# Kernel tuning notes

Measured on AMD Instinct MI355X. Metric: run time of the kernel, lower is better.

The kernel has to match this reference:

```python
import jax, jax.numpy as jnp
import numpy as np
from math import sqrt

H = 16  # head_num


def setup_inputs() -> dict:
    key = jax.random.key(0)
    ks = jax.random.split(key, 8)
    B, Sq, Skv, Dq, Dkv, Dall = 2, 2048, 2048, 1024, 1024, 1024
    x = jax.random.normal(ks[0], (B, Sq, Dq), dtype=jnp.float32)
    y = jax.random.normal(ks[1], (B, Skv, Dkv), dtype=jnp.float32)
    attention_mask = jnp.ones((B, 1, Sq, Skv), dtype=jnp.int32)
    # torch nn.Linear weights are [out, in]
    Wq = jax.random.normal(ks[2], (Dall, Dq), dtype=jnp.float32) * 0.02
    Wk = jax.random.normal(ks[3], (Dall, Dkv), dtype=jnp.float32) * 0.02
    Wv = jax.random.normal(ks[4], (Dall, Dkv), dtype=jnp.float32) * 0.02
    Wo = jax.random.normal(ks[5], (Dq, Dall), dtype=jnp.float32) * 0.02
    bo = jnp.zeros((Dq,), dtype=jnp.float32)
    return {"x": x, "y": y, "attention_mask": attention_mask,
            "Wq": Wq, "Wk": Wk, "Wv": Wv, "Wo": Wo, "bo": bo}


def reference(x, y, attention_mask, Wq, Wk, Wv, Wo, bo):
    B, Sq, _ = x.shape
    Dall = Wq.shape[0]
    Dh = Dall // H
    # projections (torch Linear: x @ W.T), split heads -> [B, H, S, Dh]
    q = (x @ Wq.T).reshape(B, Sq, H, Dh).transpose(0, 2, 1, 3)
    k = (y @ Wk.T).reshape(B, -1, H, Dh).transpose(0, 2, 1, 3)
    v = (y @ Wv.T).reshape(B, -1, H, Dh).transpose(0, 2, 1, 3)
    scores = jnp.einsum('bhqd,bhkd->bhqk', q, k)  # [B,H,Sq,Skv]
    mask = (attention_mask == 0)  # masked_fill where mask.eq(0) -> but torch does mask.eq(0) then fills True positions
    scores = jnp.where(mask, jnp.float32(-1e9), scores)
    # NOTE: faithful quirk - mask applied before scaling; scale uses sqrt(h_size)
    attn = jax.nn.softmax(scores / sqrt(Dh), axis=-1)
    out = jnp.einsum('bhqk,bhkd->bhqd', attn, v)
    out = out.transpose(0, 2, 1, 3).reshape(B, Sq, Dall)
    return out @ Wo.T + bo
```

## Files before the change

kernel.cpp:

```cpp
#include <hip/hip_runtime.h>
#include <stdint.h>


typedef __attribute__((ext_vector_type(8))) short bf16x8;
typedef __attribute__((ext_vector_type(4))) float f32x4;
typedef __attribute__((ext_vector_type(16))) float f32x16;
typedef __attribute__((ext_vector_type(2))) unsigned int u32x2;

#define LOG2E 1.44269504088896f
#define QSCALE (0.125f * LOG2E)

static __device__ __forceinline__ unsigned short f2bf(float f) {
  union { float f; unsigned int u; } v; v.f = f;
  unsigned int r = v.u + 0x7FFFu + ((v.u >> 16) & 1u);
  return (unsigned short)(r >> 16);
}

static __device__ __forceinline__ void g2l16(const void* gsrc, void* ldst) {
  __builtin_amdgcn_global_load_lds((const __attribute__((address_space(1))) unsigned int*)gsrc,
                                   (__attribute__((address_space(3))) unsigned int*)ldst,
                                   16, 0, 0);
}

static __device__ __forceinline__ unsigned int cvt_pk_bf16(float lo, float hi) {
  unsigned int r;
  asm("v_cvt_pk_bf16_f32 %0, %1, %2" : "=v"(r) : "v"(lo), "v"(hi));
  return r;
}

static __device__ __forceinline__ u32x2 pl32swap(unsigned int a, unsigned int b) {
  return __builtin_amdgcn_permlane32_swap(a, b, false, false);
}

static __device__ __forceinline__ f32x16 mfma32(bf16x8 a, bf16x8 b, f32x16 c) {
  return __builtin_amdgcn_mfma_f32_32x32x16_bf16(a, b, c, 0, 0, 0);
}

static __device__ __forceinline__ size_t kfrag_addr(int row, int col) {
  int b = row >> 11, s = row & 2047;
  int h = col >> 6, d = col & 63;
  int t32 = s >> 5, r31 = s & 31;
  int ks = d >> 4, r5 = (d >> 3) & 1, e = d & 7;
  return (size_t)(b * 16 + h) * 131072 + (size_t)t32 * 2048 + ks * 512 + (r5 * 32 + r31) * 8 + e;
}
static __device__ __forceinline__ size_t vfrag_addr(int row, int col) {
  int b = row >> 11, s = row & 2047;
  int h = col >> 6, d = col & 63;
  int t64 = s >> 6, k2 = (s >> 4) & 3, r5 = (s >> 3) & 1, e = s & 7;
  int mb = d >> 5, r31 = d & 31;
  return (size_t)(b * 16 + h) * 131072 + (size_t)t64 * 4096 + (mb * 4 + k2) * 512 + (r5 * 32 + r31) * 8 + e;
}

__global__ void k_prep(const float* __restrict__ x, const float* __restrict__ y,
                       const float* __restrict__ Wq, const float* __restrict__ Wk,
                       const float* __restrict__ Wv, const float* __restrict__ Wo,
                       const int* __restrict__ mask,
                       unsigned short* __restrict__ xb, unsigned short* __restrict__ yb,
                       unsigned short* __restrict__ Wqb, unsigned short* __restrict__ Wkb,
                       unsigned short* __restrict__ Wvb, unsigned short* __restrict__ Wob,
                       unsigned long long* __restrict__ bits, unsigned int* __restrict__ flag) {
  const int task = blockIdx.y;
  if (task == 6) {
    const int lane = threadIdx.x & 63;
    int gw = blockIdx.x * 4 + (threadIdx.x >> 6);
    bool any0 = false;
    for (; gw < 131072; gw += 4096) {
      int m = mask[(size_t)gw * 64 + lane];
      unsigned long long bal = __ballot(m != 0);
      if (lane == 0) {
        bits[gw] = bal;
        any0 |= (bal != ~0ull);
      }
    }
    if (lane == 0 && any0) atomicAnd(flag, 0u);
    return;
  }
  const float* in; unsigned short* out; int n;
  switch (task) {
    case 0: in = x;  out = xb;  n = 4194304; break;
    case 1: in = y;  out = yb;  n = 4194304; break;
    case 2: in = Wq; out = Wqb; n = 1048576; break;
    case 3: in = Wk; out = Wkb; n = 1048576; break;
    case 4: in = Wv; out = Wvb; n = 1048576; break;
    default: in = Wo; out = Wob; n = 1048576; break;
  }
  int i = (blockIdx.x * blockDim.x + threadIdx.x) * 4;
  const int stride = gridDim.x * blockDim.x * 4;
  for (; i < n; i += stride) {
    float4 v = *reinterpret_cast<const float4*>(in + i);
    ushort4 o;
    o.x = f2bf(v.x); o.y = f2bf(v.y); o.z = f2bf(v.z); o.w = f2bf(v.w);
    *reinterpret_cast<ushort4*>(out + i) = o;
  }
}

template <int OM>
static __device__ __forceinline__ void gemm_body(const unsigned short* __restrict__ A,
                                                 const unsigned short* __restrict__ W,
                                                 void* __restrict__ Cout,
                                                 const float* __restrict__ bias,
                                                 float scale) {
  __shared__ __align__(16) unsigned short As[128 * 32];
  __shared__ __align__(16) unsigned short Bs[128 * 32];
  const int tid = threadIdx.x;
  const int w = tid >> 6, lane = tid & 63;
  const int wr = w >> 1, wc = w & 1;
  const int l15 = lane & 15, lg = lane >> 4;
  const int bm = blockIdx.x, bn = blockIdx.y;

  f32x4 acc[4][4] = {};

  const int e0 = w * 1024 + lane * 8;
  const int e1 = e0 + 512;
  const int r0 = e0 >> 5, c0 = e0 & 31;
  const int r1 = e1 >> 5, c1 = e1 & 31;
  const unsigned short* A0 = A + (size_t)(bm * 128 + r0) * 1024 + c0;
  const unsigned short* A1 = A + (size_t)(bm * 128 + r1) * 1024 + c1;
  const unsigned short* W0 = W + (size_t)(bn * 128 + r0) * 1024 + c0;
  const unsigned short* W1 = W + (size_t)(bn * 128 + r1) * 1024 + c1;

  for (int kt = 0; kt < 1024; kt += 32) {
    g2l16(A0 + kt, (char*)As + e0 * 2);
    g2l16(A1 + kt, (char*)As + e1 * 2);
    g2l16(W0 + kt, (char*)Bs + e0 * 2);
    g2l16(W1 + kt, (char*)Bs + e1 * 2);
    __syncthreads();
    bf16x8 a[4], b[4];
#pragma unroll
    for (int mi = 0; mi < 4; ++mi)
      a[mi] = *reinterpret_cast<const bf16x8*>(As + (wr * 64 + mi * 16 + l15) * 32 + lg * 8);
#pragma unroll
    for (int ni = 0; ni < 4; ++ni)
      b[ni] = *reinterpret_cast<const bf16x8*>(Bs + (wc * 64 + ni * 16 + l15) * 32 + lg * 8);
#pragma unroll
    for (int mi = 0; mi < 4; ++mi)
#pragma unroll
      for (int ni = 0; ni < 4; ++ni)
        acc[mi][ni] = __builtin_amdgcn_mfma_f32_16x16x32_bf16(a[mi], b[ni], acc[mi][ni], 0, 0, 0);
    __syncthreads();
  }

#pragma unroll
  for (int ni = 0; ni < 4; ++ni) {
    const int gcol = bn * 128 + wc * 64 + ni * 16 + l15;
    float bv = (OM == 1) ? bias[gcol] : 0.f;
#pragma unroll
    for (int mi = 0; mi < 4; ++mi) {
#pragma unroll
      for (int r = 0; r < 4; ++r) {
        const int grow = bm * 128 + wr * 64 + mi * 16 + lg * 4 + r;
        if (OM == 0)
          ((unsigned short*)Cout)[(size_t)grow * 1024 + gcol] = f2bf(acc[mi][ni][r]);
        else if (OM == 1)
          ((float*)Cout)[(size_t)grow * 1024 + gcol] = acc[mi][ni][r] + bv;
        else if (OM == 2)
          ((unsigned short*)Cout)[kfrag_addr(grow, gcol)] = f2bf(acc[mi][ni][r] * scale);
        else
          ((unsigned short*)Cout)[vfrag_addr(grow, gcol)] = f2bf(acc[mi][ni][r]);
      }
    }
  }
}

__global__ __launch_bounds__(256) void k_gemm_qkv(
    const unsigned short* __restrict__ xb, const unsigned short* __restrict__ yb,
    const unsigned short* __restrict__ Wq, const unsigned short* __restrict__ Wk,
    const unsigned short* __restrict__ Wv,
    unsigned short* __restrict__ Qf, unsigned short* __restrict__ Kf,
    unsigned short* __restrict__ Vf) {
  const int z = blockIdx.z;
  if (z == 0) gemm_body<2>(xb, Wq, Qf, nullptr, QSCALE);
  else if (z == 1) gemm_body<2>(yb, Wk, Kf, nullptr, 1.f);
  else gemm_body<3>(yb, Wv, Vf, nullptr, 1.f);
}

__global__ __launch_bounds__(256) void k_gemm_o(
    const unsigned short* __restrict__ AO, const unsigned short* __restrict__ Wo,
    float* __restrict__ out, const float* __restrict__ bo) {
  gemm_body<1>(AO, Wo, out, bo, 1.f);
}


#define BUILD_PB2(SP, K2, IDX) {                                   \
    unsigned int c0_ = cvt_pk_bf16(SP[(K2)*8 + 0], SP[(K2)*8 + 1]);\
    unsigned int c1_ = cvt_pk_bf16(SP[(K2)*8 + 2], SP[(K2)*8 + 3]);\
    unsigned int c2_ = cvt_pk_bf16(SP[(K2)*8 + 4], SP[(K2)*8 + 5]);\
    unsigned int c3_ = cvt_pk_bf16(SP[(K2)*8 + 6], SP[(K2)*8 + 7]);\
    u32x2 r0_ = pl32swap(c0_, c2_);                                \
    u32x2 r1_ = pl32swap(c1_, c3_);                                \
    union { unsigned int u[4]; bf16x8 v; } f_;                     \
    f_.u[0] = r0_.x; f_.u[1] = r1_.x; f_.u[2] = r0_.y; f_.u[3] = r1_.y; \
    pb[IDX] = f_.v; }

#define STAGE_TILE(T, BUF) {                                                  \
    const size_t toff_ = (size_t)(T) * 8192;                                  \
    char* kb_ = smem + (BUF) * 16384;                                         \
    const int o0_ = (w * 2 + 0) * 1024 + lane * 16;                           \
    const int o1_ = (w * 2 + 1) * 1024 + lane * 16;                           \
    g2l16(Kg + toff_ + o0_, kb_ + o0_);                                       \
    g2l16(Kg + toff_ + o1_, kb_ + o1_);                                       \
    g2l16(Vg + toff_ + o0_, kb_ + 8192 + o0_);                                \
    g2l16(Vg + toff_ + o1_, kb_ + 8192 + o1_);                                \
  }

__global__ __launch_bounds__(256, 2) void k_attn(
    const unsigned short* __restrict__ Qf, const unsigned short* __restrict__ Kf,
    const unsigned short* __restrict__ Vf, const unsigned long long* __restrict__ bits,
    const unsigned int* __restrict__ flag, unsigned short* __restrict__ AO) {
  __shared__ __align__(16) char smem[32768];
  const int tid = threadIdx.x, w = tid >> 6, lane = tid & 63;
  const int l31 = lane & 31, hi = lane >> 5;
  const int bid = blockIdx.x;
  const int xcd = bid & 7, rr = bid >> 3;
  const int j = rr & 15;
  const int g = xcd + ((rr >> 4) << 3);
  const int h = g & 15, b = g >> 4;
  const int q = j * 128 + w * 32 + l31;
  const bool allfull = (*flag == 0xFFFFFFFFu);
  const f32x16 z16 = {};

  const size_t bh = (size_t)(b * 16 + h) * 131072;
  bf16x8 qf[4];
  const unsigned short* Qp = Qf + bh + (size_t)(j * 4 + w) * 2048 + lane * 8;
#pragma unroll
  for (int ks = 0; ks < 4; ++ks)
    qf[ks] = *reinterpret_cast<const bf16x8*>(Qp + ks * 512);

  const char* Kg = (const char*)(Kf + bh);
  const char* Vg = (const char*)(Vf + bh);
  const unsigned long long* brow = bits + (size_t)(b * 2048 + q) * 32;

  f32x16 o0 = {}, o1 = {};
  float l_run = 0.f;

  STAGE_TILE(0, 0)
  __syncthreads();

  for (int t = 0; t < 32; ++t) {
    const int cur = t & 1;
    if (t < 31) STAGE_TILE(t + 1, cur ^ 1)
    const char* Kb = smem + cur * 16384;
    const char* Vb = Kb + 8192;

    bf16x8 kf[8], vf[8];
#pragma unroll
    for (int f = 0; f < 8; ++f)
      kf[f] = *reinterpret_cast<const bf16x8*>(Kb + f * 1024 + lane * 16);

    f32x16 s0 = z16, s1 = z16;
#pragma unroll
    for (int ks = 0; ks < 4; ++ks) {
      s0 = mfma32(kf[ks], qf[ks], s0);
      s1 = mfma32(kf[4 + ks], qf[ks], s1);
    }

#pragma unroll
    for (int f = 0; f < 8; ++f)
      vf[f] = *reinterpret_cast<const bf16x8*>(Vb + f * 1024 + lane * 16);

    if (!allfull) {
      unsigned long long wb = brow[t];
      if (!__all(wb == ~0ull)) {
#pragma unroll
        for (int r = 0; r < 16; ++r) {
          const int kl = (r & 3) + 8 * (r >> 2) + 4 * hi;
          s0[r] = ((wb >> kl) & 1ull) ? s0[r] : -1e9f;
          s1[r] = ((wb >> (kl + 32)) & 1ull) ? s1[r] : -1e9f;
        }
      }
    }

#pragma unroll
    for (int r = 0; r < 16; ++r) {
      s0[r] = __builtin_amdgcn_exp2f(s0[r]);
      s1[r] = __builtin_amdgcn_exp2f(s1[r]);
    }
    {
      float sm[8];
#pragma unroll
      for (int r = 0; r < 8; ++r) sm[r] = (s0[r] + s0[r + 8]) + (s1[r] + s1[r + 8]);
      sm[0] += sm[4]; sm[1] += sm[5]; sm[2] += sm[6]; sm[3] += sm[7];
      sm[0] += sm[2]; sm[1] += sm[3];
      float ls = sm[0] + sm[1];
      u32x2 sw = pl32swap(__builtin_bit_cast(unsigned int, ls),
                          __builtin_bit_cast(unsigned int, ls));
      l_run += __builtin_bit_cast(float, sw.x) + __builtin_bit_cast(float, sw.y);
    }

    bf16x8 pb[4];
    BUILD_PB2(s0, 0, 0) BUILD_PB2(s0, 1, 1) BUILD_PB2(s1, 0, 2) BUILD_PB2(s1, 1, 3)
#pragma unroll
    for (int k2 = 0; k2 < 4; ++k2) {
      o0 = mfma32(vf[k2], pb[k2], o0);
      o1 = mfma32(vf[4 + k2], pb[k2], o1);
    }
    __syncthreads();
  }

  const float inv = 1.f / l_run;
  unsigned short* Orow = AO + (size_t)(b * 2048 + q) * 1024 + h * 64;
#pragma unroll
  for (int g2 = 0; g2 < 4; ++g2) {
    ushort4 pk;
    pk.x = f2bf(o0[g2 * 4 + 0] * inv);
    pk.y = f2bf(o0[g2 * 4 + 1] * inv);
    pk.z = f2bf(o0[g2 * 4 + 2] * inv);
    pk.w = f2bf(o0[g2 * 4 + 3] * inv);
    *reinterpret_cast<ushort4*>(Orow + 8 * g2 + 4 * hi) = pk;
    pk.x = f2bf(o1[g2 * 4 + 0] * inv);
    pk.y = f2bf(o1[g2 * 4 + 1] * inv);
    pk.z = f2bf(o1[g2 * 4 + 2] * inv);
    pk.w = f2bf(o1[g2 * 4 + 3] * inv);
    *reinterpret_cast<ushort4*>(Orow + 32 + 8 * g2 + 4 * hi) = pk;
  }
}

extern "C" void kernel_launch(void* const* d_in, const int* in_sizes, int n_in,
                              void* d_out, int out_size, void* d_ws, size_t ws_size,
                              hipStream_t stream) {
  const float* x  = (const float*)d_in[0];
  const float* y  = (const float*)d_in[1];
  const int* mask = (const int*)d_in[2];
  const float* Wq = (const float*)d_in[3];
  const float* Wk = (const float*)d_in[4];
  const float* Wv = (const float*)d_in[5];
  const float* Wo = (const float*)d_in[6];
  const float* bo = (const float*)d_in[7];

  char* ws = (char*)d_ws;
  const size_t MB = 1ull << 20;
  unsigned short* xb  = (unsigned short*)(ws + 0 * MB);
  unsigned short* yb  = (unsigned short*)(ws + 8 * MB);
  unsigned short* Wqb = (unsigned short*)(ws + 16 * MB);
  unsigned short* Wkb = (unsigned short*)(ws + 18 * MB);
  unsigned short* Wvb = (unsigned short*)(ws + 20 * MB);
  unsigned short* Wob = (unsigned short*)(ws + 22 * MB);
  unsigned short* Qf  = (unsigned short*)(ws + 24 * MB);
  unsigned short* Kf  = (unsigned short*)(ws + 32 * MB);
  unsigned short* Vf  = (unsigned short*)(ws + 40 * MB);
  unsigned short* AOb = (unsigned short*)(ws + 56 * MB);
  unsigned long long* bits = (unsigned long long*)(ws + 64 * MB);
  unsigned int* flag = (unsigned int*)(ws + 65 * MB);

  hipMemsetAsync(flag, 0xFF, 4, stream);
  k_prep<<<dim3(1024, 7), 256, 0, stream>>>(x, y, Wq, Wk, Wv, Wo, mask,
                                            xb, yb, Wqb, Wkb, Wvb, Wob, bits, flag);
  k_gemm_qkv<<<dim3(32, 8, 3), 256, 0, stream>>>(xb, yb, Wqb, Wkb, Wvb, Qf, Kf, Vf);
  k_attn<<<512, 256, 0, stream>>>(Qf, Kf, Vf, bits, flag, AOb);
  k_gemm_o<<<dim3(32, 8, 1), 256, 0, stream>>>(AOb, Wob, (float*)d_out, bo);
}
```

Before: 131.1 us.

## Fuse K and V projections sharing A tile; shrink output GEMM M-tile

K and V projections now run in one block that loads the shared y tile once and multiplies it against both Wk and Wv, removing a redundant A-tile load and one third of the QKV grid. Each KV block holds two accumulator sets, which raises register pressure and can cut occupancy. The output projection now uses 64x128 tiles with each wave covering 32 columns, doubling the grid to 512 blocks so the CUs are better filled.

```diff
diff --git a/kernel.cpp b/kernel.cpp
--- a/kernel.cpp
+++ b/kernel.cpp
@@ -94,14 +94,10 @@
   }
 }
 
-template <int OM>
-static __device__ __forceinline__ void gemm_body(const unsigned short* __restrict__ A,
-                                                 const unsigned short* __restrict__ W,
-                                                 void* __restrict__ Cout,
-                                                 const float* __restrict__ bias,
-                                                 float scale) {
-  __shared__ __align__(16) unsigned short As[128 * 32];
-  __shared__ __align__(16) unsigned short Bs[128 * 32];
+static __device__ __forceinline__ void gemm_q_core(
+    const unsigned short* __restrict__ A, const unsigned short* __restrict__ W,
+    unsigned short* __restrict__ Cout, float scale,
+    unsigned short* As, unsigned short* Bs) {
   const int tid = threadIdx.x;
   const int w = tid >> 6, lane = tid & 63;
   const int wr = w >> 1, wc = w & 1;
@@ -143,20 +139,78 @@
 #pragma unroll
   for (int ni = 0; ni < 4; ++ni) {
     const int gcol = bn * 128 + wc * 64 + ni * 16 + l15;
-    float bv = (OM == 1) ? bias[gcol] : 0.f;
 #pragma unroll
     for (int mi = 0; mi < 4; ++mi) {
 #pragma unroll
       for (int r = 0; r < 4; ++r) {
         const int grow = bm * 128 + wr * 64 + mi * 16 + lg * 4 + r;
-        if (OM == 0)
-          ((unsigned short*)Cout)[(size_t)grow * 1024 + gcol] = f2bf(acc[mi][ni][r]);
-        else if (OM == 1)
-          ((float*)Cout)[(size_t)grow * 1024 + gcol] = acc[mi][ni][r] + bv;
-        else if (OM == 2)
-          ((unsigned short*)Cout)[kfrag_addr(grow, gcol)] = f2bf(acc[mi][ni][r] * scale);
-        else
-          ((unsigned short*)Cout)[vfrag_addr(grow, gcol)] = f2bf(acc[mi][ni][r]);
+        Cout[kfrag_addr(grow, gcol)] = f2bf(acc[mi][ni][r] * scale);
+      }
+    }
+  }
+}
+
+static __device__ __forceinline__ void gemm_kv_core(
+    const unsigned short* __restrict__ A, const unsigned short* __restrict__ Wk,
+    const unsigned short* __restrict__ Wv,
+    unsigned short* __restrict__ Kf, unsigned short* __restrict__ Vf,
+    unsigned short* As, unsigned short* B0s, unsigned short* B1s) {
+  const int tid = threadIdx.x;
+  const int w = tid >> 6, lane = tid & 63;
+  const int wr = w >> 1, wc = w & 1;
+  const int l15 = lane & 15, lg = lane >> 4;
+  const int bm = blockIdx.x, bn = blockIdx.y;
+
+  f32x4 acck[4][4] = {}, accv[4][4] = {};
+
+  const int e0 = w * 1024 + lane * 8;
+  const int e1 = e0 + 512;
+  const int r0 = e0 >> 5, c0 = e0 & 31;
+  const int r1 = e1 >> 5, c1 = e1 & 31;
+  const unsigned short* A0 = A + (size_t)(bm * 128 + r0) * 1024 + c0;
+  const unsigned short* A1 = A + (size_t)(bm * 128 + r1) * 1024 + c1;
+  const unsigned short* K0 = Wk + (size_t)(bn * 128 + r0) * 1024 + c0;
+  const unsigned short* K1 = Wk + (size_t)(bn * 128 + r1) * 1024 + c1;
+  const unsigned short* V0 = Wv + (size_t)(bn * 128 + r0) * 1024 + c0;
+  const unsigned short* V1 = Wv + (size_t)(bn * 128 + r1) * 1024 + c1;
+
+  for (int kt = 0; kt < 1024; kt += 32) {
+    g2l16(A0 + kt, (char*)As + e0 * 2);
+    g2l16(A1 + kt, (char*)As + e1 * 2);
+    g2l16(K0 + kt, (char*)B0s + e0 * 2);
+    g2l16(K1 + kt, (char*)B0s + e1 * 2);
+    g2l16(V0 + kt, (char*)B1s + e0 * 2);
+    g2l16(V1 + kt, (char*)B1s + e1 * 2);
+    __syncthreads();
+    bf16x8 a[4], bk[4], bv[4];
+#pragma unroll
+    for (int mi = 0; mi < 4; ++mi)
+      a[mi] = *reinterpret_cast<const bf16x8*>(As + (wr * 64 + mi * 16 + l15) * 32 + lg * 8);
+#pragma unroll
+    for (int ni = 0; ni < 4; ++ni) {
+      bk[ni] = *reinterpret_cast<const bf16x8*>(B0s + (wc * 64 + ni * 16 + l15) * 32 + lg * 8);
+      bv[ni] = *reinterpret_cast<const bf16x8*>(B1s + (wc * 64 + ni * 16 + l15) * 32 + lg * 8);
+    }
+#pragma unroll
+    for (int mi = 0; mi < 4; ++mi)
+#pragma unroll
+      for (int ni = 0; ni < 4; ++ni) {
+        acck[mi][ni] = __builtin_amdgcn_mfma_f32_16x16x32_bf16(a[mi], bk[ni], acck[mi][ni], 0, 0, 0);
+        accv[mi][ni] = __builtin_amdgcn_mfma_f32_16x16x32_bf16(a[mi], bv[ni], accv[mi][ni], 0, 0, 0);
+      }
+    __syncthreads();
+  }
+
+#pragma unroll
+  for (int ni = 0; ni < 4; ++ni) {
+    const int gcol = bn * 128 + wc * 64 + ni * 16 + l15;
+#pragma unroll
+    for (int mi = 0; mi < 4; ++mi) {
+#pragma unroll
+      for (int r = 0; r < 4; ++r) {
+        const int grow = bm * 128 + wr * 64 + mi * 16 + lg * 4 + r;
+        Kf[kfrag_addr(grow, gcol)] = f2bf(acck[mi][ni][r]);
+        Vf[vfrag_addr(grow, gcol)] = f2bf(accv[mi][ni][r]);
       }
     }
   }
@@ -168,16 +222,68 @@
     const unsigned short* __restrict__ Wv,
     unsigned short* __restrict__ Qf, unsigned short* __restrict__ Kf,
     unsigned short* __restrict__ Vf) {
-  const int z = blockIdx.z;
-  if (z == 0) gemm_body<2>(xb, Wq, Qf, nullptr, QSCALE);
-  else if (z == 1) gemm_body<2>(yb, Wk, Kf, nullptr, 1.f);
-  else gemm_body<3>(yb, Wv, Vf, nullptr, 1.f);
+  __shared__ __align__(16) unsigned short As[128 * 32];
+  __shared__ __align__(16) unsigned short B0s[128 * 32];
+  __shared__ __align__(16) unsigned short B1s[128 * 32];
+  if (blockIdx.z == 0) gemm_q_core(xb, Wq, Qf, QSCALE, As, B0s);
+  else gemm_kv_core(yb, Wk, Wv, Kf, Vf, As, B0s, B1s);
 }
 
 __global__ __launch_bounds__(256) void k_gemm_o(
-    const unsigned short* __restrict__ AO, const unsigned short* __restrict__ Wo,
+    const unsigned short* __restrict__ A, const unsigned short* __restrict__ W,
     float* __restrict__ out, const float* __restrict__ bo) {
-  gemm_body<1>(AO, Wo, out, bo, 1.f);
+  __shared__ __align__(16) unsigned short As[64 * 32];
+  __shared__ __align__(16) unsigned short Bs[128 * 32];
+  const int tid = threadIdx.x;
+  const int w = tid >> 6, lane = tid & 63;
+  const int l15 = lane & 15, lg = lane >> 4;
+  const int bm = blockIdx.x, bn = blockIdx.y;
+
+  f32x4 acc[4][2] = {};
+
+  const int ea = tid * 8;
+  const int eb0 = tid * 8;
+  const int eb1 = eb0 + 2048;
+  const int ra = ea >> 5, ca = ea & 31;
+  const int rb0 = eb0 >> 5, cb0 = eb0 & 31;
+  const int rb1 = eb1 >> 5, cb1 = eb1 & 31;
+  const unsigned short* A0 = A + (size_t)(bm * 64 + ra) * 1024 + ca;
+  const unsigned short* W0 = W + (size_t)(bn * 128 + rb0) * 1024 + cb0;
+  const unsigned short* W1 = W + (size_t)(bn * 128 + rb1) * 1024 + cb1;
+
+  for (int kt = 0; kt < 1024; kt += 32) {
+    g2l16(A0 + kt, (char*)As + ea * 2);
+    g2l16(W0 + kt, (char*)Bs + eb0 * 2);
+    g2l16(W1 + kt, (char*)Bs + eb1 * 2);
+    __syncthreads();
+    bf16x8 a[4], b[2];
+#pragma unroll
+    for (int mi = 0; mi < 4; ++mi)
+      a[mi] = *reinterpret_cast<const bf16x8*>(As + (mi * 16 + l15) * 32 + lg * 8);
+#pragma unroll
+    for (int ni = 0; ni < 2; ++ni)
+      b[ni] = *reinterpret_cast<const bf16x8*>(Bs + (w * 32 + ni * 16 + l15) * 32 + lg * 8);
+#pragma unroll
+    for (int mi = 0; mi < 4; ++mi)
+#pragma unroll
+      for (int ni = 0; ni < 2; ++ni)
+        acc[mi][ni] = __builtin_amdgcn_mfma_f32_16x16x32_bf16(a[mi], b[ni], acc[mi][ni], 0, 0, 0);
+    __syncthreads();
+  }
+
+#pragma unroll
+  for (int ni = 0; ni < 2; ++ni) {
+    const int gcol = bn * 128 + w * 32 + ni * 16 + l15;
+    const float bv = bo[gcol];
+#pragma unroll
+    for (int mi = 0; mi < 4; ++mi) {
+#pragma unroll
+      for (int r = 0; r < 4; ++r) {
+        const int grow = bm * 64 + mi * 16 + lg * 4 + r;
+        out[(size_t)grow * 1024 + gcol] = acc[mi][ni][r] + bv;
+      }
+    }
+  }
 }
 
 
@@ -345,7 +451,7 @@
   hipMemsetAsync(flag, 0xFF, 4, stream);
   k_prep<<<dim3(1024, 7), 256, 0, stream>>>(x, y, Wq, Wk, Wv, Wo, mask,
                                             xb, yb, Wqb, Wkb, Wvb, Wob, bits, flag);
-  k_gemm_qkv<<<dim3(32, 8, 3), 256, 0, stream>>>(xb, yb, Wqb, Wkb, Wvb, Qf, Kf, Vf);
+  k_gemm_qkv<<<dim3(32, 8, 2), 256, 0, stream>>>(xb, yb, Wqb, Wkb, Wvb, Qf, Kf, Vf);
   k_attn<<<512, 256, 0, stream>>>(Qf, Kf, Vf, bits, flag, AOb);
-  k_gemm_o<<<dim3(32, 8, 1), 256, 0, stream>>>(AOb, Wob, (float*)d_out, bo);
-}
+  k_gemm_o<<<dim3(64, 8), 256, 0, stream>>>(AOb, Wob, (float*)d_out, bo);
+}
```

After: 154.6 us. +17.9%, slower.
